# Kernel optimization log

Hardware: AMD Instinct MI355X
Metric: run time of the kernel (lower is better)

Reference implementation:

```python
import jax, jax.numpy as jnp
import numpy as np

IN_FEATURES = 8192
OUT_FEATURES = 8192
BITS = 4
TILE = 16
M_TOKENS = 64  # small token count -> dequant-traffic dominated (memory regime)
SCALE_BLOCK = 128


def setup_inputs() -> dict:
    key = jax.random.key(0)
    k1, k2, k3, k4, k5, k6 = jax.random.split(key, 6)
    tiles_k = IN_FEATURES // TILE
    tiles_n = OUT_FEATURES // TILE
    packed_bytes = 256 * BITS // 8  # 128 bytes per 16x16 tile for 4-bit
    x = jax.random.normal(k1, (M_TOKENS, IN_FEATURES), dtype=jnp.float32)
    packed_indices = jax.random.randint(k2, (tiles_k, tiles_n, packed_bytes), 0, 256, dtype=jnp.int32)
    scales = jax.random.uniform(k3, ((IN_FEATURES + SCALE_BLOCK - 1) // SCALE_BLOCK, OUT_FEATURES), dtype=jnp.float32, minval=0.5, maxval=1.5)
    su = jax.random.normal(k4, (IN_FEATURES,), dtype=jnp.float32)
    sv = jax.random.normal(k5, (OUT_FEATURES,), dtype=jnp.float32)
    grid = jax.random.normal(k6, (2 ** BITS,), dtype=jnp.float32)  # trellis codebook grid
    return {"x": x, "packed_indices": packed_indices, "scales": scales, "su": su, "sv": sv, "grid": grid}


def _dequantize(packed_indices, scales, su, sv, grid):
    # packed_indices: [tiles_k, tiles_n, packed_bytes] byte values (0..255)
    tk, tn, pb = packed_indices.shape
    bits = (pb * 8) // (TILE * TILE)
    # unpack bytes -> bits (little-endian within byte), then group into bits-per-index
    bitplane = (packed_indices[..., None] >> jnp.arange(8, dtype=jnp.int32)) & 1  # [tk, tn, pb, 8]
    idx = (bitplane.reshape(tk, tn, TILE * TILE, bits)
           * (2 ** jnp.arange(bits, dtype=jnp.int32))).sum(-1)  # [tk, tn, 256]
    vals = grid[idx].reshape(tk, tn, TILE, TILE)  # tile element order: (k_in_tile, n_in_tile)
    # assemble full weight laid out [K_in, N_out]
    W = vals.transpose(0, 2, 1, 3).reshape(tk * TILE, tn * TILE)
    # per-128-row-block scales over the K dim
    nb = scales.shape[0]
    W = (W.reshape(nb, SCALE_BLOCK, tn * TILE) * scales[:, None, :]).reshape(tk * TILE, tn * TILE)
    # per-row (su) and per-column (sv) scale/sign vectors
    W = W * su[:, None] * sv[None, :]
    return W  # [in_features, out_features]


def reference(x, packed_indices, scales, su, sv, grid):
    W = _dequantize(packed_indices, scales, su, sv, grid)  # [K, N]
    # torch: x.view(-1, K) @ weights[N, K].T  ==  x @ W[K, N]
    lead = x.shape[:-1]
    out = x.reshape(-1, W.shape[0]) @ W
    return out.reshape(*lead, W.shape[1])
```

## Files before the change

### kernel.cpp

```cpp
#include <hip/hip_runtime.h>

typedef float f32x4 __attribute__((ext_vector_type(4)));
typedef __bf16 bf16x8 __attribute__((ext_vector_type(8)));

#define K_FEAT 8192
#define N_FEAT 8192
#define M_TOK 64
#define TILES_N 512
#define TILES_K 512
#define WROWSTRIDE 40
#define LG_KSPLIT 3
#define KSPLIT 8
#define NSTEP 32

__device__ __forceinline__ unsigned short f2bf(float f) {
    unsigned int u = __builtin_bit_cast(unsigned int, f);
    u = (u + 0x7FFFu + ((u >> 16) & 1u)) >> 16;
    return (unsigned short)u;
}
__device__ __forceinline__ float bf2f(unsigned short h) {
    return __builtin_bit_cast(float, (unsigned int)h << 16);
}

__global__ void __launch_bounds__(256)
prep_x_kernel(const float* __restrict__ x, const float* __restrict__ su,
              unsigned short* __restrict__ xb)
{
    int i = blockIdx.x * 256 + threadIdx.x;
    const float4* x4 = (const float4*)x;
    const float4* su4 = (const float4*)su;
    float4 xv = x4[i];
    float4 s4 = su4[i & (K_FEAT / 4 - 1)];
    ushort4 o;
    o.x = f2bf(xv.x * s4.x);
    o.y = f2bf(xv.y * s4.y);
    o.z = f2bf(xv.z * s4.z);
    o.w = f2bf(xv.w * s4.w);
    ((ushort4*)xb)[i] = o;
}

__global__ void __launch_bounds__(256)
trellis_main(const int* __restrict__ packed,
             const float* __restrict__ scales,
             const float* __restrict__ sv,
             const float* __restrict__ grid,
             const unsigned short* __restrict__ xb,
             unsigned short* __restrict__ partials)
{
    __shared__ unsigned int table[256];
    __shared__ unsigned short wlds[2][64 * WROWSTRIDE];
    __shared__ float slds[8 * 64];

    const int tid = threadIdx.x;
    const int bid = blockIdx.x;
    const int s = bid & (KSPLIT - 1);
    const int ng = bid >> LG_KSPLIT;
    const int col0 = ng * 64;
    const int nt0 = ng * 4;
    const int ktile0 = s * (TILES_K / KSPLIT);

    const int tau = tid >> 5;
    const int dkt = tau >> 2;
    const int dnt = tau & 3;
    const int l32 = tid & 31;
    const int q = l32 >> 1;
    const int r = l32 & 1;

    const int* pb = packed
        + ((size_t)(ktile0 + dkt) * TILES_N + (nt0 + dnt)) * 128 + 4 * l32;
    const int stepstride = 2 * TILES_N * 128;

    const int wave = tid >> 6;
    const int lane = tid & 63;
    const int ln15 = lane & 15;
    const int kgrp = (lane >> 4) * 8;
    const unsigned short* xrow = xb + (size_t)(wave * 16 + ln15) * K_FEAT;

    {
        float lo = grid[tid & 15];
        float hi = grid[(tid >> 4) & 15];
        table[tid] = (unsigned int)f2bf(lo) | ((unsigned int)f2bf(hi) << 16);
    }
    {
        const int kb0 = s * 8;
        slds[tid]       = scales[(size_t)(kb0 + (tid >> 6)) * N_FEAT + col0 + (tid & 63)];
        slds[tid + 256] = scales[(size_t)(kb0 + 4 + (tid >> 6)) * N_FEAT + col0 + (tid & 63)];
    }

    uint4 a = *(const uint4*)(pb);
    uint4 ra = *(const uint4*)(xrow + ktile0 * 16 + kgrp);

    f32x4 acc[4], acc2[4];
    for (int d = 0; d < 4; ++d)
        for (int j = 0; j < 4; ++j) { acc[d][j] = 0.f; acc2[d][j] = 0.f; }

    __syncthreads();

    for (int t = 0; t < NSTEP; ++t) {
        const int tc = (t + 1 < NSTEP) ? (t + 1) : t;
        uint4 nx = *(const uint4*)(pb + (size_t)tc * stepstride);

        uint4 wq;
        wq.x = table[a.x & 255];
        wq.y = table[a.y & 255];
        wq.z = table[a.z & 255];
        wq.w = table[a.w & 255];
        {
            unsigned short* ws0 =
                &wlds[t & 1][(dnt * 16 + 8 * r) * WROWSTRIDE + dkt * 16 + q];
            ws0[0 * WROWSTRIDE] = (unsigned short)(wq.x);
            ws0[1 * WROWSTRIDE] = (unsigned short)(wq.x >> 16);
            ws0[2 * WROWSTRIDE] = (unsigned short)(wq.y);
            ws0[3 * WROWSTRIDE] = (unsigned short)(wq.y >> 16);
            ws0[4 * WROWSTRIDE] = (unsigned short)(wq.z);
            ws0[5 * WROWSTRIDE] = (unsigned short)(wq.z >> 16);
            ws0[6 * WROWSTRIDE] = (unsigned short)(wq.w);
            ws0[7 * WROWSTRIDE] = (unsigned short)(wq.w >> 16);
        }

        __builtin_amdgcn_sched_barrier(0);
        asm volatile("s_waitcnt lgkmcnt(0)" ::: "memory");
        __builtin_amdgcn_s_barrier();
        __builtin_amdgcn_sched_barrier(0);

        int k0n = ktile0 * 16 + (t + 1 < NSTEP ? (t + 1) : 0) * 32;
        uint4 ran = *(const uint4*)(xrow + k0n + kgrp);

        bf16x8 aa = __builtin_bit_cast(bf16x8, ra);
        const unsigned short* wbase = &wlds[t & 1][0];
        for (int d = 0; d < 4; ++d) {
            bf16x8 b = *(const bf16x8*)(wbase + (d * 16 + ln15) * WROWSTRIDE + kgrp);
            acc2[d] = __builtin_amdgcn_mfma_f32_16x16x32_bf16(aa, b, acc2[d], 0, 0, 0);
        }
        ra = ran;
        a = nx;

        if ((t & 3) == 3) {
            const float* srow = slds + (t >> 2) * 64 + ln15;
            for (int d = 0; d < 4; ++d) {
                float sc = srow[d * 16];
                acc[d] += acc2[d] * sc;
                for (int j = 0; j < 4; ++j) acc2[d][j] = 0.f;
            }
        }
    }

    unsigned short* pout = partials + (size_t)s * (M_TOK * N_FEAT);
    const int rbase = (lane >> 4) * 4;
    for (int d = 0; d < 4; ++d) {
        int n = col0 + d * 16 + ln15;
        float svv = sv[n];
        for (int j = 0; j < 4; ++j) {
            int m = wave * 16 + rbase + j;
            pout[(size_t)m * N_FEAT + n] = f2bf(acc[d][j] * svv);
        }
    }
}

__global__ void __launch_bounds__(256)
reduce_kernel(const unsigned short* __restrict__ partials, float* __restrict__ out)
{
    int i = blockIdx.x * 256 + threadIdx.x;
    const uint4* p = (const uint4*)partials;
    float acc[8];
    for (int e = 0; e < 8; ++e) acc[e] = 0.f;
    for (int k = 0; k < KSPLIT; ++k) {
        uint4 v = p[(size_t)k * (M_TOK * N_FEAT / 8) + i];
        unsigned int uu[4] = {v.x, v.y, v.z, v.w};
        for (int q = 0; q < 4; ++q) {
            acc[2 * q]     += bf2f((unsigned short)(uu[q] & 0xFFFFu));
            acc[2 * q + 1] += bf2f((unsigned short)(uu[q] >> 16));
        }
    }
    float4 o0 = make_float4(acc[0], acc[1], acc[2], acc[3]);
    float4 o1 = make_float4(acc[4], acc[5], acc[6], acc[7]);
    ((float4*)out)[2 * i]     = o0;
    ((float4*)out)[2 * i + 1] = o1;
}

extern "C" void kernel_launch(void* const* d_in, const int* in_sizes, int n_in,
                              void* d_out, int out_size, void* d_ws, size_t ws_size,
                              hipStream_t stream)
{
    const float* x      = (const float*)d_in[0];
    const int*   packed = (const int*)d_in[1];
    const float* scales = (const float*)d_in[2];
    const float* su     = (const float*)d_in[3];
    const float* sv     = (const float*)d_in[4];
    const float* grid   = (const float*)d_in[5];
    float* out = (float*)d_out;

    unsigned short* xb = (unsigned short*)d_ws;
    const size_t xb_bytes = (size_t)M_TOK * K_FEAT * 2;
    unsigned short* partials = (unsigned short*)((char*)d_ws + xb_bytes);

    prep_x_kernel<<<(M_TOK * K_FEAT / 4) / 256, 256, 0, stream>>>(x, su, xb);
    trellis_main<<<(N_FEAT / 64) * KSPLIT, 256, 0, stream>>>(
        packed, scales, sv, grid, xb, partials);
    reduce_kernel<<<(M_TOK * N_FEAT / 8) / 256, 256, 0, stream>>>(partials, out);
}
```

Measured before the change: 39.44 us.

## Give each wave its own N-tile to remove per-step block barriers

Each wave now dequantizes and consumes its own 16-column weight tile in a private double-buffered LDS region, so the per-step s_waitcnt plus block-wide s_barrier is removed. Each wave loops over all four 16-row M blocks of activations instead of four N tiles. The packed-weight prefetch is deepened to two steps ahead. The cost is four activation loads per step per wave instead of one, which means more register pressure and more global and L2 traffic for x. The code also relies on intra-wave LDS ordering for the write-then-read handoff, with no explicit wait before the read.

```diff
diff --git a/kernel.cpp b/kernel.cpp
--- a/kernel.cpp
+++ b/kernel.cpp
@@ -8,7 +8,7 @@
 #define M_TOK 64
 #define TILES_N 512
 #define TILES_K 512
-#define WROWSTRIDE 40
+#define WROW 40
 #define LG_KSPLIT 3
 #define KSPLIT 8
 #define NSTEP 32
@@ -48,7 +48,7 @@
              unsigned short* __restrict__ partials)
 {
     __shared__ unsigned int table[256];
-    __shared__ unsigned short wlds[2][64 * WROWSTRIDE];
+    __shared__ unsigned short wlds[4][2][16 * WROW];
     __shared__ float slds[8 * 64];
 
     const int tid = threadIdx.x;
@@ -59,22 +59,25 @@
     const int nt0 = ng * 4;
     const int ktile0 = s * (TILES_K / KSPLIT);
 
-    const int tau = tid >> 5;
-    const int dkt = tau >> 2;
-    const int dnt = tau & 3;
-    const int l32 = tid & 31;
+    const int wn = tid >> 6;
+    const int lane = tid & 63;
+    const int l5 = lane >> 5;
+    const int l32 = lane & 31;
     const int q = l32 >> 1;
     const int r = l32 & 1;
-
-    const int* pb = packed
-        + ((size_t)(ktile0 + dkt) * TILES_N + (nt0 + dnt)) * 128 + 4 * l32;
-    const int stepstride = 2 * TILES_N * 128;
-
-    const int wave = tid >> 6;
-    const int lane = tid & 63;
     const int ln15 = lane & 15;
     const int kgrp = (lane >> 4) * 8;
-    const unsigned short* xrow = xb + (size_t)(wave * 16 + ln15) * K_FEAT;
+
+    const int* pb = packed
+        + ((size_t)(ktile0 + l5) * TILES_N + (nt0 + wn)) * 128 + 4 * l32;
+    const int stepstride = 2 * TILES_N * 128;
+
+    const int wo = (8 * r) * WROW + l5 * 16 + q;
+    const int ro = ln15 * WROW + kgrp;
+    unsigned short* buf0 = &wlds[wn][0][0];
+    unsigned short* buf1 = &wlds[wn][1][0];
+
+    const unsigned short* xbase = xb + (size_t)ln15 * K_FEAT + ktile0 * 16 + kgrp;
 
     {
         float lo = grid[tid & 15];
@@ -86,72 +89,101 @@
         slds[tid]       = scales[(size_t)(kb0 + (tid >> 6)) * N_FEAT + col0 + (tid & 63)];
         slds[tid + 256] = scales[(size_t)(kb0 + 4 + (tid >> 6)) * N_FEAT + col0 + (tid & 63)];
     }
-
-    uint4 a = *(const uint4*)(pb);
-    uint4 ra = *(const uint4*)(xrow + ktile0 * 16 + kgrp);
+    __syncthreads();
+
+    uint4 pk0    = *(const uint4*)(pb);
+    uint4 pk_nxt = *(const uint4*)(pb + stepstride);
+    uint4 ac0 = *(const uint4*)(xbase);
+    uint4 ac1 = *(const uint4*)(xbase + 16 * K_FEAT);
+    uint4 ac2 = *(const uint4*)(xbase + 32 * K_FEAT);
+    uint4 ac3 = *(const uint4*)(xbase + 48 * K_FEAT);
+    {
+        uint4 wq;
+        wq.x = table[pk0.x & 255];
+        wq.y = table[pk0.y & 255];
+        wq.z = table[pk0.z & 255];
+        wq.w = table[pk0.w & 255];
+        unsigned short* wp = buf0 + wo;
+        wp[0 * WROW] = (unsigned short)(wq.x);
+        wp[1 * WROW] = (unsigned short)(wq.x >> 16);
+        wp[2 * WROW] = (unsigned short)(wq.y);
+        wp[3 * WROW] = (unsigned short)(wq.y >> 16);
+        wp[4 * WROW] = (unsigned short)(wq.z);
+        wp[5 * WROW] = (unsigned short)(wq.z >> 16);
+        wp[6 * WROW] = (unsigned short)(wq.w);
+        wp[7 * WROW] = (unsigned short)(wq.w >> 16);
+    }
 
     f32x4 acc[4], acc2[4];
+#pragma unroll
     for (int d = 0; d < 4; ++d)
+#pragma unroll
         for (int j = 0; j < 4; ++j) { acc[d][j] = 0.f; acc2[d][j] = 0.f; }
 
-    __syncthreads();
+    unsigned short* brd = buf0;
+    unsigned short* bw  = buf1;
 
     for (int t = 0; t < NSTEP; ++t) {
-        const int tc = (t + 1 < NSTEP) ? (t + 1) : t;
-        uint4 nx = *(const uint4*)(pb + (size_t)tc * stepstride);
-
-        uint4 wq;
-        wq.x = table[a.x & 255];
-        wq.y = table[a.y & 255];
-        wq.z = table[a.z & 255];
-        wq.w = table[a.w & 255];
+        const int t2 = (t + 2 < NSTEP) ? t + 2 : NSTEP - 1;
+        uint4 pk_fut = *(const uint4*)(pb + (size_t)t2 * stepstride);
+        const int t1 = (t + 1 < NSTEP) ? t + 1 : NSTEP - 1;
+        const unsigned short* xn = xbase + t1 * 32;
+        uint4 an0 = *(const uint4*)(xn);
+        uint4 an1 = *(const uint4*)(xn + 16 * K_FEAT);
+        uint4 an2 = *(const uint4*)(xn + 32 * K_FEAT);
+        uint4 an3 = *(const uint4*)(xn + 48 * K_FEAT);
+
         {
-            unsigned short* ws0 =
-                &wlds[t & 1][(dnt * 16 + 8 * r) * WROWSTRIDE + dkt * 16 + q];
-            ws0[0 * WROWSTRIDE] = (unsigned short)(wq.x);
-            ws0[1 * WROWSTRIDE] = (unsigned short)(wq.x >> 16);
-            ws0[2 * WROWSTRIDE] = (unsigned short)(wq.y);
-            ws0[3 * WROWSTRIDE] = (unsigned short)(wq.y >> 16);
-            ws0[4 * WROWSTRIDE] = (unsigned short)(wq.z);
-            ws0[5 * WROWSTRIDE] = (unsigned short)(wq.z >> 16);
-            ws0[6 * WROWSTRIDE] = (unsigned short)(wq.w);
-            ws0[7 * WROWSTRIDE] = (unsigned short)(wq.w >> 16);
-        }
-
-        __builtin_amdgcn_sched_barrier(0);
-        asm volatile("s_waitcnt lgkmcnt(0)" ::: "memory");
-        __builtin_amdgcn_s_barrier();
-        __builtin_amdgcn_sched_barrier(0);
-
-        int k0n = ktile0 * 16 + (t + 1 < NSTEP ? (t + 1) : 0) * 32;
-        uint4 ran = *(const uint4*)(xrow + k0n + kgrp);
-
-        bf16x8 aa = __builtin_bit_cast(bf16x8, ra);
-        const unsigned short* wbase = &wlds[t & 1][0];
-        for (int d = 0; d < 4; ++d) {
-            bf16x8 b = *(const bf16x8*)(wbase + (d * 16 + ln15) * WROWSTRIDE + kgrp);
-            acc2[d] = __builtin_amdgcn_mfma_f32_16x16x32_bf16(aa, b, acc2[d], 0, 0, 0);
-        }
-        ra = ran;
-        a = nx;
+            uint4 wq;
+            wq.x = table[pk_nxt.x & 255];
+            wq.y = table[pk_nxt.y & 255];
+            wq.z = table[pk_nxt.z & 255];
+            wq.w = table[pk_nxt.w & 255];
+            unsigned short* wp = bw + wo;
+            wp[0 * WROW] = (unsigned short)(wq.x);
+            wp[1 * WROW] = (unsigned short)(wq.x >> 16);
+            wp[2 * WROW] = (unsigned short)(wq.y);
+            wp[3 * WROW] = (unsigned short)(wq.y >> 16);
+            wp[4 * WROW] = (unsigned short)(wq.z);
+            wp[5 * WROW] = (unsigned short)(wq.z >> 16);
+            wp[6 * WROW] = (unsigned short)(wq.w);
+            wp[7 * WROW] = (unsigned short)(wq.w >> 16);
+        }
+
+        bf16x8 bfrag = *(const bf16x8*)(brd + ro);
+        acc2[0] = __builtin_amdgcn_mfma_f32_16x16x32_bf16(
+            __builtin_bit_cast(bf16x8, ac0), bfrag, acc2[0], 0, 0, 0);
+        acc2[1] = __builtin_amdgcn_mfma_f32_16x16x32_bf16(
+            __builtin_bit_cast(bf16x8, ac1), bfrag, acc2[1], 0, 0, 0);
+        acc2[2] = __builtin_amdgcn_mfma_f32_16x16x32_bf16(
+            __builtin_bit_cast(bf16x8, ac2), bfrag, acc2[2], 0, 0, 0);
+        acc2[3] = __builtin_amdgcn_mfma_f32_16x16x32_bf16(
+            __builtin_bit_cast(bf16x8, ac3), bfrag, acc2[3], 0, 0, 0);
 
         if ((t & 3) == 3) {
-            const float* srow = slds + (t >> 2) * 64 + ln15;
+            float sc = slds[(t >> 2) * 64 + wn * 16 + ln15];
+#pragma unroll
             for (int d = 0; d < 4; ++d) {
-                float sc = srow[d * 16];
                 acc[d] += acc2[d] * sc;
+#pragma unroll
                 for (int j = 0; j < 4; ++j) acc2[d][j] = 0.f;
             }
         }
+
+        pk_nxt = pk_fut;
+        ac0 = an0; ac1 = an1; ac2 = an2; ac3 = an3;
+        unsigned short* tmp = brd; brd = bw; bw = tmp;
     }
 
     unsigned short* pout = partials + (size_t)s * (M_TOK * N_FEAT);
+    const int n = col0 + wn * 16 + ln15;
+    const float svv = sv[n];
     const int rbase = (lane >> 4) * 4;
+#pragma unroll
     for (int d = 0; d < 4; ++d) {
-        int n = col0 + d * 16 + ln15;
-        float svv = sv[n];
+#pragma unroll
         for (int j = 0; j < 4; ++j) {
-            int m = wave * 16 + rbase + j;
+            int m = d * 16 + rbase + j;
             pout[(size_t)m * N_FEAT + n] = f2bf(acc[d][j] * svv);
         }
     }
```

New measurement: 76.44 us. 93.8% more time.
